# Optimization experiments

Measured on AMD Instinct MI355X. Metric: run time of the kernel, lower is better.

Reference implementation:

```python
import jax, jax.numpy as jnp
import numpy as np

N_HEADS = 32
N_KV = 8
HEAD_DIM = 128
ROPE_THETA = 10000.0
PAST_LEN = 2048


def _rope_cos_sin(position_ids):
    # inv_freq: [head_dim/2]
    inv_freq = 1.0 / (ROPE_THETA ** (jnp.arange(0, HEAD_DIM, 2, dtype=jnp.float32) / HEAD_DIM))
    freqs = position_ids.astype(jnp.float32)[..., None] * inv_freq  # [B, S, hd/2]
    emb = jnp.concatenate([freqs, freqs], axis=-1)  # [B, S, hd]
    return jnp.cos(emb), jnp.sin(emb)


def _rotate_half(x):
    x1, x2 = jnp.split(x, 2, axis=-1)
    return jnp.concatenate([-x2, x1], axis=-1)


def setup_inputs() -> dict:
    key = jax.random.key(0)
    ks = jax.random.split(key, 10)
    B, S = 1, 2048
    IN = 8192
    s = 0.02
    return {
        "hidden_states": jax.random.normal(ks[0], (B, S, IN), jnp.float32),
        "position_ids": (jnp.arange(S, dtype=jnp.int32) + PAST_LEN)[None, :],
        "cache_k": jax.random.normal(ks[1], (B, N_KV, PAST_LEN, HEAD_DIM), jnp.float32),
        "cache_v": jax.random.normal(ks[2], (B, N_KV, PAST_LEN, HEAD_DIM), jnp.float32),
        "Wq": jax.random.normal(ks[3], (N_HEADS * HEAD_DIM, IN), jnp.float32) * s,
        "bq": jax.random.normal(ks[4], (N_HEADS * HEAD_DIM,), jnp.float32) * s,
        "Wk": jax.random.normal(ks[5], (N_KV * HEAD_DIM, IN), jnp.float32) * s,
        "bk": jax.random.normal(ks[6], (N_KV * HEAD_DIM,), jnp.float32) * s,
        "Wv": jax.random.normal(ks[7], (N_KV * HEAD_DIM, IN), jnp.float32) * s,
        "bv": jax.random.normal(ks[8], (N_KV * HEAD_DIM,), jnp.float32) * s,
        "Wo": jax.random.normal(ks[9], (N_HEADS * HEAD_DIM, N_HEADS * HEAD_DIM), jnp.float32) * s,
    }


def reference(hidden_states, position_ids, cache_k, cache_v, Wq, bq, Wk, bk, Wv, bv, Wo):
    B, Sq, _ = hidden_states.shape
    G = N_HEADS // N_KV

    # QKV projections -> [B, H, S, D]
    q = (hidden_states @ Wq.T + bq).reshape(B, Sq, N_HEADS, HEAD_DIM).transpose(0, 2, 1, 3)
    k = (hidden_states @ Wk.T + bk).reshape(B, Sq, N_KV, HEAD_DIM).transpose(0, 2, 1, 3)
    v = (hidden_states @ Wv.T + bv).reshape(B, Sq, N_KV, HEAD_DIM).transpose(0, 2, 1, 3)

    # RoPE
    cos, sin = _rope_cos_sin(position_ids)  # [B, Sq, D]
    cos, sin = cos[:, None], sin[:, None]   # broadcast over heads
    q = q * cos + _rotate_half(q) * sin
    k = k * cos + _rotate_half(k) * sin

    # KV cache concat
    key = jnp.concatenate([cache_k, k], axis=2)   # [B, Kv, Sk, D]
    value = jnp.concatenate([cache_v, v], axis=2)
    Sk = key.shape[2]
    past_len = Sk - Sq

    # GQA attention (grouped einsum == repeat_interleave + SDPA)
    qg = q.reshape(B, N_KV, G, Sq, HEAD_DIM)
    scale = 1.0 / jnp.sqrt(jnp.float32(HEAD_DIM))
    scores = jnp.einsum("bkgqd,bkld->bkgql", qg, key) * scale  # [B, Kv, G, Sq, Sk]

    q_pos = past_len + jnp.arange(Sq)
    mask = jnp.arange(Sk)[None, :] <= q_pos[:, None]  # [Sq, Sk]
    scores = jnp.where(mask[None, None, None], scores, -jnp.inf)
    attn = jax.nn.softmax(scores, axis=-1)

    ctx = jnp.einsum("bkgql,bkld->bkgqd", attn, value)
    ctx = ctx.reshape(B, N_HEADS, Sq, HEAD_DIM).transpose(0, 2, 1, 3).reshape(B, Sq, N_HEADS * HEAD_DIM)
    out = ctx @ Wo.T
    return out, key, value
```

## Files before the change

kernel.cpp:

```cpp
#include <hip/hip_runtime.h>
#include <hip/hip_bf16.h>
#include <math.h>

typedef float f32x4 __attribute__((ext_vector_type(4)));
typedef short s16x8 __attribute__((ext_vector_type(8)));
typedef __bf16 bf16x8 __attribute__((ext_vector_type(8)));

__device__ __forceinline__ unsigned short f2bf(float f) {
  unsigned int u = __builtin_bit_cast(unsigned int, f);
  u += 0x7fffu + ((u >> 16) & 1u);
  return (unsigned short)(u >> 16);
}

__device__ __forceinline__ f32x4 mfma16(s16x8 a, s16x8 b, f32x4 c) {
  return __builtin_amdgcn_mfma_f32_16x16x32_bf16(
      __builtin_bit_cast(bf16x8, a), __builtin_bit_cast(bf16x8, b), c, 0, 0, 0);
}

#define GLDS(gp, lp) __builtin_amdgcn_global_load_lds(                      \
    (__attribute__((address_space(1))) void*)(gp),                          \
    (__attribute__((address_space(3))) void*)(lp), 16, 0, 0)

struct __attribute__((aligned(8))) us4 { unsigned short x, y, z, w; };
__device__ __forceinline__ us4 cvt4(float4 v) {
  us4 r; r.x = f2bf(v.x); r.y = f2bf(v.y); r.z = f2bf(v.z); r.w = f2bf(v.w);
  return r;
}

__global__ __launch_bounds__(256) void conv_all(
    const float4* __restrict__ h, const float4* __restrict__ wq,
    const float4* __restrict__ wk, const float4* __restrict__ wv,
    const float4* __restrict__ wo, const float4* __restrict__ bq,
    const float4* __restrict__ bk, const float4* __restrict__ bv,
    us4* __restrict__ hbf, us4* __restrict__ wqkvbf, us4* __restrict__ wobf,
    float4* __restrict__ biasc)
{
  const unsigned int U = 20973056u;
  const unsigned int stride = gridDim.x * blockDim.x;
  for (unsigned int u = blockIdx.x * blockDim.x + threadIdx.x; u < U; u += stride) {
    if (u < 4194304u) {
      hbf[u] = cvt4(h[u]);
    } else if (u < 12582912u) {
      unsigned int o = u - 4194304u;  wqkvbf[o] = cvt4(wq[o]);
    } else if (u < 14680064u) {
      unsigned int o = u - 12582912u; wqkvbf[8388608u + o] = cvt4(wk[o]);
    } else if (u < 16777216u) {
      unsigned int o = u - 14680064u; wqkvbf[10485760u + o] = cvt4(wv[o]);
    } else if (u < 20971520u) {
      unsigned int o = u - 16777216u; wobf[o] = cvt4(wo[o]);
    } else {
      unsigned int o = u - 20971520u;
      float4 v = (o < 1024u) ? bq[o] : (o < 1280u) ? bk[o - 1024u] : bv[o - 1280u];
      biasc[o] = v;
    }
  }
}

__global__ __launch_bounds__(256) void rope_table(const int* __restrict__ pos_ids,
                                                  float* __restrict__ cost,
                                                  float* __restrict__ sint)
{
  int idx = blockIdx.x * blockDim.x + threadIdx.x;
  if (idx >= 131072) return;
  int s = idx >> 6, i = idx & 63;
  double invf = exp(-((double)i / 64.0) * 9.210340371976184);
  double ang = (double)pos_ids[s] * invf;
  cost[idx] = (float)cos(ang);
  sint[idx] = (float)sin(ang);
}

template<int NF>
__global__ __launch_bounds__(512, 2) void gemm8p(const unsigned short* __restrict__ A,
                                                 const unsigned short* __restrict__ B,
                                                 const float* __restrict__ bias,
                                                 float* __restrict__ C,
                                                 int M, int N, int K)
{
  constexpr int BN = NF * 64;
  constexpr int BUFSZ = 32768 + BN * 128;
  __shared__ char smem[2 * BUFSZ];
  const int tid = threadIdx.x;
  const int l = tid & 63;
  const int w = tid >> 6;
  const int wm = w >> 2, wn = w & 3;
  const int wr = wm * 128;
  const int wc = wn * (16 * NF);
  const int lk16 = (l >> 4) * 16;

  const int nwg = gridDim.x;
  const int s = (blockIdx.x & 7) * (nwg >> 3) + (blockIdx.x >> 3);
  const int NBY = M >> 8;
  const int by = s % NBY, bx = s / NBY;
  const size_t arow0 = (size_t)by * 256;
  const size_t brow0 = (size_t)bx * BN;
  const size_t Kb = (size_t)K * 2;
  const char* Ab = (const char*)A;
  const char* Bb = (const char*)B;

  f32x4 acc[8][NF];
#pragma unroll
  for (int i = 0; i < 8; ++i)
#pragma unroll
    for (int j = 0; j < NF; ++j) acc[i][j] = (f32x4){0.f, 0.f, 0.f, 0.f};

  auto STAGE = [&](int t, char* buf) {
    const size_t k0b = (size_t)t * 128;
#pragma unroll
    for (int cc = 0; cc < 4; ++cc) {
      const int ch = cc * 512 + tid;
      const int r = ch >> 3;
      const int c2s = ((ch & 7) * 16) ^ ((r & 7) << 4);
      GLDS(Ab + (arow0 + r) * Kb + k0b + c2s, buf + ch * 16);
    }
#pragma unroll
    for (int cc = 0; cc < NF; ++cc) {
      const int ch = cc * 512 + tid;
      const int r = ch >> 3;
      const int c2s = ((ch & 7) * 16) ^ ((r & 7) << 4);
      GLDS(Bb + (brow0 + r) * Kb + k0b + c2s, buf + 32768 + ch * 16);
    }
  };

  const int nt = K >> 6;
  STAGE(0, smem);
  asm volatile("s_waitcnt vmcnt(0)" ::: "memory");
  __builtin_amdgcn_s_barrier();

  for (int t = 0; t < nt; ++t) {
    char* cur = smem + (t & 1) * BUFSZ;
    if (t + 1 < nt) STAGE(t + 1, smem + ((t + 1) & 1) * BUFSZ);
    s16x8 bfr[NF][2];
#pragma unroll
    for (int qd = 0; qd < 4; ++qd) {
      s16x8 afr[2][2];
#pragma unroll
      for (int i = 0; i < 2; ++i)
#pragma unroll
        for (int k = 0; k < 2; ++k) {
          const int r = wr + (qd * 2 + i) * 16 + (l & 15);
          const int c2 = k * 64 + lk16;
          afr[i][k] = *(const s16x8*)(cur + (r * 128 + (c2 ^ ((r & 7) << 4))));
        }
      if (qd == 0) {
#pragma unroll
        for (int n = 0; n < NF; ++n)
#pragma unroll
          for (int k = 0; k < 2; ++k) {
            const int r = wc + n * 16 + (l & 15);
            const int c2 = k * 64 + lk16;
            bfr[n][k] = *(const s16x8*)(cur + 32768 + (r * 128 + (c2 ^ ((r & 7) << 4))));
          }
      }
      asm volatile("" ::: "memory");
      __builtin_amdgcn_s_barrier();
      __builtin_amdgcn_s_setprio(1);
#pragma unroll
      for (int i = 0; i < 2; ++i)
#pragma unroll
        for (int n = 0; n < NF; ++n)
#pragma unroll
          for (int k = 0; k < 2; ++k)
            acc[qd * 2 + i][n] = mfma16(afr[i][k], bfr[n][k], acc[qd * 2 + i][n]);
      __builtin_amdgcn_s_setprio(0);
      asm volatile("" ::: "memory");
      __builtin_amdgcn_s_barrier();
    }
    asm volatile("s_waitcnt vmcnt(0)" ::: "memory");
    __builtin_amdgcn_s_barrier();
  }

  const int r0 = (int)arow0 + wr + (l >> 4) * 4;
  const int c0 = (int)brow0 + wc + (l & 15);
#pragma unroll
  for (int mi = 0; mi < 8; ++mi) {
#pragma unroll
    for (int ni = 0; ni < NF; ++ni) {
      const int c = c0 + ni * 16;
      const float bvv = bias ? bias[c] : 0.f;
#pragma unroll
      for (int rr = 0; rr < 4; ++rr) {
        const int r = r0 + mi * 16 + rr;
        C[(size_t)r * N + c] = acc[mi][ni][rr] + bvv;
      }
    }
  }
}

__global__ __launch_bounds__(256) void rope_scatter(
    const float* __restrict__ qkv, const float* __restrict__ cost,
    const float* __restrict__ sint, const float* __restrict__ cache_k,
    const float* __restrict__ cache_v, float* __restrict__ keyout,
    float* __restrict__ valout, unsigned short* __restrict__ qbf,
    char* __restrict__ kswz, char* __restrict__ vswz)
{
  const float rs = 0.08838834764831845f;
  const int stride = gridDim.x * blockDim.x;
  for (int idx = blockIdx.x * blockDim.x + threadIdx.x; idx < 11534336; idx += stride) {
    if (idx < 4194304) {
      int i = idx & 63, hh = (idx >> 6) & 31, s = idx >> 11;
      const float* base = qkv + (size_t)s * 6144 + hh * 128 + i;
      float q1 = base[0], q2 = base[64];
      float c = cost[s * 64 + i], sn = sint[s * 64 + i];
      float o1 = (q1 * c - q2 * sn) * rs, o2 = (q2 * c + q1 * sn) * rs;
      unsigned short* qd = qbf + ((size_t)hh * 2048 + s) * 128 + i;
      qd[0] = f2bf(o1); qd[64] = f2bf(o2);
    } else if (idx < 5242880) {
      int j = idx - 4194304;
      int i = j & 63, kh = (j >> 6) & 7, s = j >> 9;
      const float* base = qkv + (size_t)s * 6144 + 4096 + kh * 128 + i;
      float k1 = base[0], k2 = base[64];
      float c = cost[s * 64 + i], sn = sint[s * 64 + i];
      float o1 = k1 * c - k2 * sn, o2 = k2 * c + k1 * sn;
      float* kd = keyout + ((size_t)kh * 4096 + 2048 + s) * 128 + i;
      kd[0] = o1; kd[64] = o2;
      int t = 32 + (s >> 6), r = s & 63;
      char* tb = kswz + (size_t)(kh * 64 + t) * 16384;
      *(unsigned short*)(tb + ((r * 256 + i * 2) ^ ((r & 7) << 4))) = f2bf(o1);
      *(unsigned short*)(tb + ((r * 256 + (i + 64) * 2) ^ ((r & 7) << 4))) = f2bf(o2);
    } else if (idx < 7340032) {
      int j = idx - 5242880;
      int d = j & 127, kh = (j >> 7) & 7, s = j >> 10;
      float v = qkv[(size_t)s * 6144 + 5120 + kh * 128 + d];
      valout[((size_t)kh * 4096 + 2048 + s) * 128 + d] = v;
      int t = 32 + (s >> 6), c = s & 63;
      char* tb = vswz + (size_t)(kh * 64 + t) * 16384;
      *(unsigned short*)(tb + ((d * 128 + c * 2) ^ ((d & 7) << 4))) = f2bf(v);
    } else if (idx < 9437184) {
      int j = idx - 7340032;
      int d = j & 127, s = (j >> 7) & 2047, kh = j >> 18;
      float v = cache_k[(size_t)(kh * 2048 + s) * 128 + d];
      keyout[((size_t)kh * 4096 + s) * 128 + d] = v;
      int t = s >> 6, r = s & 63;
      char* tb = kswz + (size_t)(kh * 64 + t) * 16384;
      *(unsigned short*)(tb + ((r * 256 + d * 2) ^ ((r & 7) << 4))) = f2bf(v);
    } else {
      int j = idx - 9437184;
      int d = j & 127, s = (j >> 7) & 2047, kh = j >> 18;
      float v = cache_v[(size_t)(kh * 2048 + s) * 128 + d];
      valout[((size_t)kh * 4096 + s) * 128 + d] = v;
      int t = s >> 6, c = s & 63;
      char* tb = vswz + (size_t)(kh * 64 + t) * 16384;
      *(unsigned short*)(tb + ((d * 128 + c * 2) ^ ((d & 7) << 4))) = f2bf(v);
    }
  }
}

__global__ __launch_bounds__(512) void attn_fwd(const unsigned short* __restrict__ qbf,
                                                const char* __restrict__ kswz,
                                                const char* __restrict__ vswz,
                                                unsigned short* __restrict__ ctx)
{
  __shared__ char smem[81920];
  char* Ps = smem + 65536;
  const int tid = threadIdx.x;
  const int l = tid & 63;
  const int w = tid >> 6;
  const int d = blockIdx.x;
  const int b = d >> 5;
  const int qt = (b < 8) ? b : 23 - b;
  const int h = (d & 7) * 4 + ((d >> 3) & 3);
  const int kh = h >> 2;
  const int nt = 2 * qt + 34;
  const int qrow16 = (l >> 4) * 4;

  s16x8 aq[4];
  {
    const int qr = qt * 128 + w * 16 + (l & 15);
    const unsigned short* qp = qbf + ((size_t)h * 2048 + qr) * 128 + (l >> 4) * 8;
#pragma unroll
    for (int kc = 0; kc < 4; ++kc) aq[kc] = *(const s16x8*)(qp + kc * 32);
  }
  f32x4 o[8];
#pragma unroll
  for (int i = 0; i < 8; ++i) o[i] = (f32x4){0.f, 0.f, 0.f, 0.f};
  float m[4] = {-1e30f, -1e30f, -1e30f, -1e30f};
  float ls[4] = {0.f, 0.f, 0.f, 0.f};

  const char* kb0 = kswz + (size_t)kh * (64 * 16384);
  const char* vb0 = vswz + (size_t)kh * (64 * 16384);
  char* Pw = Ps + w * 2048;

  auto STAGE = [&](int t, int c) {
    const char* kb = kb0 + (size_t)t * 16384;
    const char* vb = vb0 + (size_t)t * 16384;
    char* Kt = smem + c * 32768;
    char* Vt = Kt + 16384;
#pragma unroll
    for (int j = 0; j < 2; ++j) {
      const int cw = j * 8 + w;
      GLDS(kb + (cw * 64 + l) * 16, Kt + cw * 1024);
      GLDS(vb + (cw * 64 + l) * 16, Vt + cw * 1024);
    }
  };

  STAGE(0, 0);
  int c = 0;
  for (int t = 0; t < nt; ++t) {
    const int tn = (t + 1 < nt) ? t + 1 : t;
    STAGE(tn, c ^ 1);
    asm volatile("s_waitcnt vmcnt(4)" ::: "memory");
    __builtin_amdgcn_s_barrier();
    asm volatile("" ::: "memory");
    const char* Kt = smem + c * 32768;
    const char* Vt = Kt + 16384;

    f32x4 s[4];
#pragma unroll
    for (int i = 0; i < 4; ++i) s[i] = (f32x4){0.f, 0.f, 0.f, 0.f};
    __builtin_amdgcn_s_setprio(1);
#pragma unroll
    for (int kc = 0; kc < 4; ++kc) {
      const int d0b = (kc * 32 + (l >> 4) * 8) * 2;
#pragma unroll
      for (int ni = 0; ni < 4; ++ni) {
        const int row = ni * 16 + (l & 15);
        s16x8 kf = *(const s16x8*)(Kt + ((row * 256 + d0b) ^ ((row & 7) << 4)));
        s[ni] = mfma16(aq[kc], kf, s[ni]);
      }
    }
    __builtin_amdgcn_s_setprio(0);
    if (t >= nt - 2) {
      const int qpos_b = 2048 + qt * 128 + w * 16 + qrow16;
      const int kvcol = (l & 15);
#pragma unroll
      for (int ni = 0; ni < 4; ++ni) {
        const int kvpos = t * 64 + ni * 16 + kvcol;
#pragma unroll
        for (int rr = 0; rr < 4; ++rr)
          if (kvpos > qpos_b + rr) s[ni][rr] = -1e30f;
      }
    }
    float rm[4];
#pragma unroll
    for (int rr = 0; rr < 4; ++rr)
      rm[rr] = fmaxf(fmaxf(s[0][rr], s[1][rr]), fmaxf(s[2][rr], s[3][rr]));
#pragma unroll
    for (int rr = 0; rr < 4; ++rr) {
      float v = rm[rr];
      v = fmaxf(v, __shfl_xor(v, 1));
      v = fmaxf(v, __shfl_xor(v, 2));
      v = fmaxf(v, __shfl_xor(v, 4));
      v = fmaxf(v, __shfl_xor(v, 8));
      rm[rr] = v;
    }
    const bool ok = (rm[0] <= m[0] + 8.f) && (rm[1] <= m[1] + 8.f) &&
                    (rm[2] <= m[2] + 8.f) && (rm[3] <= m[3] + 8.f);
    if (!__all(ok)) {
      float fs[4];
#pragma unroll
      for (int rr = 0; rr < 4; ++rr) {
        const float nm = fmaxf(m[rr], rm[rr]);
        fs[rr] = __expf(m[rr] - nm);
        m[rr] = nm;
      }
#pragma unroll
      for (int i = 0; i < 8; ++i)
#pragma unroll
        for (int rr = 0; rr < 4; ++rr) o[i][rr] *= fs[rr];
#pragma unroll
      for (int rr = 0; rr < 4; ++rr) ls[rr] *= fs[rr];
    }
    float rsum[4] = {0.f, 0.f, 0.f, 0.f};
#pragma unroll
    for (int ni = 0; ni < 4; ++ni)
#pragma unroll
      for (int rr = 0; rr < 4; ++rr) {
        const float p = __expf(s[ni][rr] - m[rr]);
        s[ni][rr] = p;
        rsum[rr] += p;
      }
#pragma unroll
    for (int rr = 0; rr < 4; ++rr) {
      float v = rsum[rr];
      v += __shfl_xor(v, 1);
      v += __shfl_xor(v, 2);
      v += __shfl_xor(v, 4);
      v += __shfl_xor(v, 8);
      ls[rr] += v;
    }
#pragma unroll
    for (int ni = 0; ni < 4; ++ni) {
      const int colb = (ni * 16 + (l & 15)) * 2;
#pragma unroll
      for (int rr = 0; rr < 4; ++rr) {
        const int q = qrow16 + rr;
        *(unsigned short*)(Pw + ((q * 128 + colb) ^ ((q & 7) << 4))) = f2bf(s[ni][rr]);
      }
    }
    s16x8 pa[2];
#pragma unroll
    for (int kc2 = 0; kc2 < 2; ++kc2) {
      const int q = l & 15;
      const int kvb = (kc2 * 32 + (l >> 4) * 8) * 2;
      pa[kc2] = *(const s16x8*)(Pw + ((q * 128 + kvb) ^ ((q & 7) << 4)));
    }
    __builtin_amdgcn_s_setprio(1);
#pragma unroll
    for (int sub = 0; sub < 8; ++sub) {
      const int dd = sub * 16 + (l & 15);
#pragma unroll
      for (int kc2 = 0; kc2 < 2; ++kc2) {
        const int kvb = (kc2 * 32 + (l >> 4) * 8) * 2;
        s16x8 vf = *(const s16x8*)(Vt + ((dd * 128 + kvb) ^ ((dd & 7) << 4)));
        o[sub] = mfma16(pa[kc2], vf, o[sub]);
      }
    }
    __builtin_amdgcn_s_setprio(0);
    asm volatile("" ::: "memory");
    __builtin_amdgcn_s_barrier();
    c ^= 1;
  }
  asm volatile("s_waitcnt vmcnt(0)" ::: "memory");

  const int r0 = qt * 128 + w * 16 + qrow16;
  const int c0 = h * 128 + (l & 15);
#pragma unroll
  for (int sub = 0; sub < 8; ++sub)
#pragma unroll
    for (int rr = 0; rr < 4; ++rr) {
      const float v = o[sub][rr] / ls[rr];
      ctx[(size_t)(r0 + rr) * 4096 + c0 + sub * 16] = f2bf(v);
    }
}

extern "C" void kernel_launch(void* const* d_in, const int* in_sizes, int n_in,
                              void* d_out, int out_size, void* d_ws, size_t ws_size,
                              hipStream_t stream) {
  (void)in_sizes; (void)n_in; (void)out_size; (void)ws_size;
  const float* hs     = (const float*)d_in[0];
  const int*   pos    = (const int*)d_in[1];
  const float* cachek = (const float*)d_in[2];
  const float* cachev = (const float*)d_in[3];
  const float* Wq     = (const float*)d_in[4];
  const float* bq     = (const float*)d_in[5];
  const float* Wk     = (const float*)d_in[6];
  const float* bk     = (const float*)d_in[7];
  const float* Wv     = (const float*)d_in[8];
  const float* bv     = (const float*)d_in[9];
  const float* Wo     = (const float*)d_in[10];

  float* out    = (float*)d_out;
  float* keyout = out + (size_t)2048 * 4096;
  float* valout = keyout + (size_t)8 * 4096 * 128;

  char* ws = (char*)d_ws;
  unsigned short* hbf    = (unsigned short*)(ws + 0);
  unsigned short* qbf    = (unsigned short*)(ws + 0);
  char*           kswz   = ws + 16777216;
  char*           vswz   = ws + 25165824;
  unsigned short* wqkvbf = (unsigned short*)(ws + 33554432);
  unsigned short* wobf   = (unsigned short*)(ws + 134217728);
  float*          qkvf   = (float*)(ws + 167772160);
  unsigned short* ctxbf  = (unsigned short*)(ws + 167772160);
  float*          cost   = (float*)(ws + 218103808);
  float*          sint   = (float*)(ws + 218628096);
  float*          biasc  = (float*)(ws + 219152384);

  conv_all<<<2048, 256, 0, stream>>>((const float4*)hs, (const float4*)Wq,
                                     (const float4*)Wk, (const float4*)Wv,
                                     (const float4*)Wo, (const float4*)bq,
                                     (const float4*)bk, (const float4*)bv,
                                     (us4*)hbf, (us4*)wqkvbf, (us4*)wobf,
                                     (float4*)biasc);
  rope_table<<<512, 256, 0, stream>>>(pos, cost, sint);
  gemm8p<3><<<256, 512, 0, stream>>>(hbf, wqkvbf, biasc, qkvf, 2048, 6144, 8192);
  rope_scatter<<<2048, 256, 0, stream>>>(qkvf, cost, sint, cachek, cachev,
                                         keyout, valout, qbf, kswz, vswz);
  attn_fwd<<<512, 512, 0, stream>>>(qbf, kswz, vswz, ctxbf);
  gemm8p<2><<<256, 512, 0, stream>>>(ctxbf, wobf, nullptr, out, 2048, 4096, 4096);
}
```

Measured before the change: 668.3 us.

## Restructure attention loop: single barrier, exp2 softmax, deferred row-sum reduction

The attention inner loop now waits for all loads and issues the next tile's prefetch after the barrier, which lets it drop the trailing per-iteration barrier. The softmax uses exp2 with a pre-scaled max and fuses the exponentiation into the P write. The per-row sum is kept per lane and reduced across lanes only once at the end, where the division becomes a reciprocal multiply. Float-to-bf16 conversion switches to the hardware cast. The loads now have less overlap with compute, since the wait is vmcnt(0) just before the next stage is issued.

```diff
diff --git a/kernel.cpp b/kernel.cpp
--- a/kernel.cpp
+++ b/kernel.cpp
@@ -7,9 +7,7 @@
 typedef __bf16 bf16x8 __attribute__((ext_vector_type(8)));
 
 __device__ __forceinline__ unsigned short f2bf(float f) {
-  unsigned int u = __builtin_bit_cast(unsigned int, f);
-  u += 0x7fffu + ((u >> 16) & 1u);
-  return (unsigned short)(u >> 16);
+  return __builtin_bit_cast(unsigned short, (__bf16)f);
 }
 
 __device__ __forceinline__ f32x4 mfma16(s16x8 a, s16x8 b, f32x4 c) {
@@ -262,6 +260,7 @@
   const int kh = h >> 2;
   const int nt = 2 * qt + 34;
   const int qrow16 = (l >> 4) * 4;
+  const float L2E = 1.44269504f;
 
   s16x8 aq[4];
   {
@@ -273,7 +272,8 @@
   f32x4 o[8];
 #pragma unroll
   for (int i = 0; i < 8; ++i) o[i] = (f32x4){0.f, 0.f, 0.f, 0.f};
-  float m[4] = {-1e30f, -1e30f, -1e30f, -1e30f};
+  float m[4]  = {-1e30f, -1e30f, -1e30f, -1e30f};
+  float m2[4] = {-1e30f, -1e30f, -1e30f, -1e30f};
   float ls[4] = {0.f, 0.f, 0.f, 0.f};
 
   const char* kb0 = kswz + (size_t)kh * (64 * 16384);
@@ -296,11 +296,10 @@
   STAGE(0, 0);
   int c = 0;
   for (int t = 0; t < nt; ++t) {
-    const int tn = (t + 1 < nt) ? t + 1 : t;
-    STAGE(tn, c ^ 1);
-    asm volatile("s_waitcnt vmcnt(4)" ::: "memory");
+    asm volatile("s_waitcnt vmcnt(0)" ::: "memory");
     __builtin_amdgcn_s_barrier();
     asm volatile("" ::: "memory");
+    if (t + 1 < nt) STAGE(t + 1, c ^ 1);
     const char* Kt = smem + c * 32768;
     const char* Vt = Kt + 16384;
 
@@ -350,8 +349,9 @@
 #pragma unroll
       for (int rr = 0; rr < 4; ++rr) {
         const float nm = fmaxf(m[rr], rm[rr]);
-        fs[rr] = __expf(m[rr] - nm);
+        fs[rr] = __builtin_amdgcn_exp2f((m[rr] - nm) * L2E);
         m[rr] = nm;
+        m2[rr] = nm * L2E;
       }
 #pragma unroll
       for (int i = 0; i < 8; ++i)
@@ -359,32 +359,16 @@
         for (int rr = 0; rr < 4; ++rr) o[i][rr] *= fs[rr];
 #pragma unroll
       for (int rr = 0; rr < 4; ++rr) ls[rr] *= fs[rr];
-    }
-    float rsum[4] = {0.f, 0.f, 0.f, 0.f};
-#pragma unroll
-    for (int ni = 0; ni < 4; ++ni)
-#pragma unroll
-      for (int rr = 0; rr < 4; ++rr) {
-        const float p = __expf(s[ni][rr] - m[rr]);
-        s[ni][rr] = p;
-        rsum[rr] += p;
-      }
-#pragma unroll
-    for (int rr = 0; rr < 4; ++rr) {
-      float v = rsum[rr];
-      v += __shfl_xor(v, 1);
-      v += __shfl_xor(v, 2);
-      v += __shfl_xor(v, 4);
-      v += __shfl_xor(v, 8);
-      ls[rr] += v;
     }
 #pragma unroll
     for (int ni = 0; ni < 4; ++ni) {
       const int colb = (ni * 16 + (l & 15)) * 2;
 #pragma unroll
       for (int rr = 0; rr < 4; ++rr) {
+        const float p = __builtin_amdgcn_exp2f(__builtin_fmaf(s[ni][rr], L2E, -m2[rr]));
+        ls[rr] += p;
         const int q = qrow16 + rr;
-        *(unsigned short*)(Pw + ((q * 128 + colb) ^ ((q & 7) << 4))) = f2bf(s[ni][rr]);
+        *(__bf16*)(Pw + ((q * 128 + colb) ^ ((q & 7) << 4))) = (__bf16)p;
       }
     }
     s16x8 pa[2];
@@ -407,18 +391,25 @@
     }
     __builtin_amdgcn_s_setprio(0);
     asm volatile("" ::: "memory");
-    __builtin_amdgcn_s_barrier();
     c ^= 1;
   }
-  asm volatile("s_waitcnt vmcnt(0)" ::: "memory");
-
+
+#pragma unroll
+  for (int rr = 0; rr < 4; ++rr) {
+    float v = ls[rr];
+    v += __shfl_xor(v, 1);
+    v += __shfl_xor(v, 2);
+    v += __shfl_xor(v, 4);
+    v += __shfl_xor(v, 8);
+    ls[rr] = 1.0f / v;
+  }
   const int r0 = qt * 128 + w * 16 + qrow16;
   const int c0 = h * 128 + (l & 15);
 #pragma unroll
   for (int sub = 0; sub < 8; ++sub)
 #pragma unroll
     for (int rr = 0; rr < 4; ++rr) {
-      const float v = o[sub][rr] / ls[rr];
+      const float v = o[sub][rr] * ls[rr];
       ctx[(size_t)(r0 + rr) * 4096 + c0 + sub * 16] = f2bf(v);
     }
 }
```

Result: faster. 637.0 us (-4.7%).
